# Kernel optimization log

Measured on AMD Instinct MI355X. Metric: run time of the kernel, lower is better.

The kernel has to match this reference:

```python
import jax, jax.numpy as jnp
import numpy as np
import math

B, C, N = 16, 512, 2048
MID = C // 2
EPS = 1e-5

def setup_inputs() -> dict:
    key = jax.random.key(0)
    ks = jax.random.split(key, 16)
    s = 0.02
    return {
        "x": jax.random.normal(ks[0], (B, C, N), jnp.float32),
        "wq": jax.random.normal(ks[1], (MID, C), jnp.float32) * s,
        "bq": jnp.zeros((MID,), jnp.float32),
        "gq": jnp.ones((MID,), jnp.float32),
        "betaq": jnp.zeros((MID,), jnp.float32),
        "wk": jax.random.normal(ks[2], (MID, C), jnp.float32) * s,
        "bk": jnp.zeros((MID,), jnp.float32),
        "gk": jnp.ones((MID,), jnp.float32),
        "betak": jnp.zeros((MID,), jnp.float32),
        "wv": jax.random.normal(ks[3], (MID, C), jnp.float32) * s,
        "bv": jnp.zeros((MID,), jnp.float32),
        "wo": jax.random.normal(ks[4], (C, MID), jnp.float32) * s,
        "bo": jnp.zeros((C,), jnp.float32),
        "mq": jnp.zeros((MID,), jnp.float32),
        "vq": jnp.ones((MID,), jnp.float32),
        "mk": jnp.zeros((MID,), jnp.float32),
        "vk": jnp.ones((MID,), jnp.float32),
    }

def _proj(x, w, b):
    # 1x1 Conv1d == per-position linear: [mid, C] x [B, C, N] -> [B, mid, N]
    return jnp.einsum('mc,bcn->bmn', w, x) + b[None, :, None]

def _bn_relu(z, gamma, beta, mean, var):
    # eval-mode BatchNorm1d over channel axis, then ReLU
    inv = gamma / jnp.sqrt(var + EPS)
    return jax.nn.relu(z * inv[None, :, None] + (beta - mean * inv)[None, :, None])

def reference(x, wq, bq, gq, betaq, wk, bk, gk, betak, wv, bv, wo, bo, mq, vq, mk, vk):
    q = _bn_relu(_proj(x, wq, bq), gq, betaq, mq, vq)   # [B, mid, N]
    k = _bn_relu(_proj(x, wk, bk), gk, betak, mk, vk)   # [B, mid, N]
    v = _proj(x, wv, bv)                                # [B, mid, N]
    scores = jnp.einsum('bmi,bmj->bij', q, k) / math.sqrt(MID)  # [B, Nq, Nk]
    attn = jax.nn.softmax(scores, axis=1)               # softmax over QUERY axis (dim=1)
    ctx = jnp.einsum('bci,bij->bcj', v, attn)           # [B, mid, N]
    out = jnp.einsum('cm,bmn->bcn', wo, ctx) + bo[None, :, None]
    return x + out
```

## Files before the change

### kernel.cpp

```cpp
#include <hip/hip_runtime.h>
#include <hip/hip_bf16.h>

#define B_ 16
#define C_ 512
#define N_ 2048
#define MID_ 256
#define EPS_ 1e-5f

typedef __attribute__((ext_vector_type(8))) short bf16x8;
typedef __attribute__((ext_vector_type(4))) float f32x4;
typedef __attribute__((ext_vector_type(8))) unsigned short us8;
typedef __attribute__((ext_vector_type(4))) unsigned short us4;

static __device__ __forceinline__ float bf2f(unsigned short u) {
    union { unsigned int i; float f; } c; c.i = ((unsigned int)u) << 16; return c.f;
}
static __device__ __forceinline__ unsigned short f2bf(float f) {
    __hip_bfloat16 h = __float2bfloat16(f);
    return *reinterpret_cast<unsigned short*>(&h);
}
static __device__ __forceinline__ us8 pack8(float4 a, float4 b) {
    us8 r;
    r[0] = f2bf(a.x); r[1] = f2bf(a.y); r[2] = f2bf(a.z); r[3] = f2bf(a.w);
    r[4] = f2bf(b.x); r[5] = f2bf(b.y); r[6] = f2bf(b.z); r[7] = f2bf(b.w);
    return r;
}

__global__ __launch_bounds__(256) void prep_x_kernel(
    const float* __restrict__ x, unsigned short* __restrict__ xt)
{
    const int b  = blockIdx.z;
    const int c0 = blockIdx.y * 64;
    const int n0 = blockIdx.x * 64;
    __shared__ unsigned short Ts[64][72];

    const int tid = threadIdx.x;
    const int cc  = tid >> 2;
    const int cq  = (tid & 3) * 4;

    #pragma unroll
    for (int i = 0; i < 4; i++) {
        float4 f = *(const float4*)&x[((size_t)b * C_ + c0 + cc) * N_ + n0 + cq + 16 * i];
        Ts[cq + 16 * i + 0][cc] = f2bf(f.x);
        Ts[cq + 16 * i + 1][cc] = f2bf(f.y);
        Ts[cq + 16 * i + 2][cc] = f2bf(f.z);
        Ts[cq + 16 * i + 3][cc] = f2bf(f.w);
    }
    __syncthreads();

    const int nn = tid >> 2;
    const int cg = (tid & 3) * 16;
    #pragma unroll
    for (int i = 0; i < 2; i++)
        *(us8*)&xt[((size_t)b * N_ + n0 + nn) * C_ + c0 + cg + 8 * i] =
            *(const us8*)&Ts[nn][cg + 8 * i];
}

__global__ __launch_bounds__(256) void prep_w_kernel(
    const float* __restrict__ wq, const float* __restrict__ wk,
    const float* __restrict__ wv, unsigned short* __restrict__ wb)
{
    const int nthr = gridDim.x * 256;
    for (int u = blockIdx.x * 256 + threadIdx.x; u < 98304; u += nthr) {
        int p = u >> 15;
        int o4 = u & 32767;
        const float* src = (p == 0) ? wq : (p == 1) ? wk : wv;
        float4 f = *(const float4*)&src[o4 * 4];
        us4 r;
        r[0] = f2bf(f.x); r[1] = f2bf(f.y); r[2] = f2bf(f.z); r[3] = f2bf(f.w);
        *(us4*)&wb[(size_t)p * 131072 + o4 * 4] = r;
    }
}

__global__ __launch_bounds__(256) void qkv_gemm_kernel(
    const unsigned short* __restrict__ xt, const unsigned short* __restrict__ wb,
    const float* __restrict__ bq, const float* __restrict__ gq,
    const float* __restrict__ betaq, const float* __restrict__ mq,
    const float* __restrict__ vq,
    const float* __restrict__ bk, const float* __restrict__ gk,
    const float* __restrict__ betak, const float* __restrict__ mk,
    const float* __restrict__ vk,
    const float* __restrict__ bv,
    unsigned short* __restrict__ qt, unsigned short* __restrict__ kt,
    unsigned short* __restrict__ v)
{
    const int p  = blockIdx.z % 3;
    const int b  = blockIdx.z / 3;
    const int n0 = blockIdx.x * 128;
    const int m0 = blockIdx.y * 128;

    __shared__ unsigned short Ws[128][72];
    __shared__ unsigned short Xs[128][72];
    __shared__ float sc_s[128], of_s[128];

    const int tid  = threadIdx.x;
    const int wave = tid >> 6;
    const int lane = tid & 63;
    const int quad = lane >> 4;
    const int l16  = lane & 15;
    const int wi   = wave >> 1;
    const int wj   = wave & 1;

    const unsigned short* wbp = wb + (size_t)p * 131072;
    const unsigned short* xtb = xt + (size_t)b * N_ * C_;

    if (tid < 128) {
        int m = m0 + tid;
        if (p == 0) {
            float inv = gq[m] * rsqrtf(vq[m] + EPS_);
            sc_s[tid] = inv * 0.0625f;
            of_s[tid] = ((bq[m] - mq[m]) * inv + betaq[m]) * 0.0625f;
        } else if (p == 1) {
            float inv = gk[m] * rsqrtf(vk[m] + EPS_);
            sc_s[tid] = inv; of_s[tid] = (bk[m] - mk[m]) * inv + betak[m];
        } else {
            sc_s[tid] = 1.0f; of_s[tid] = bv[m];
        }
    }

    unsigned short (*Asrc)[72] = (p == 2) ? Xs : Ws;
    unsigned short (*Bsrc)[72] = (p == 2) ? Ws : Xs;

    f32x4 acc[4][4];
    #pragma unroll
    for (int it = 0; it < 4; it++)
        #pragma unroll
        for (int jt = 0; jt < 4; jt++)
            #pragma unroll
            for (int r = 0; r < 4; r++) acc[it][jt][r] = 0.0f;

    const int srow  = tid >> 1;
    const int shalf = (tid & 1) * 32;

    for (int k0 = 0; k0 < C_; k0 += 64) {
        __syncthreads();
        #pragma unroll
        for (int i = 0; i < 4; i++) {
            *(us8*)&Ws[srow][shalf + 8 * i] =
                *(const us8*)&wbp[(size_t)(m0 + srow) * C_ + k0 + shalf + 8 * i];
            *(us8*)&Xs[srow][shalf + 8 * i] =
                *(const us8*)&xtb[(size_t)(n0 + srow) * C_ + k0 + shalf + 8 * i];
        }
        __syncthreads();
        #pragma unroll
        for (int cl = 0; cl < 64; cl += 32) {
            bf16x8 af[4], bfr[4];
            #pragma unroll
            for (int t = 0; t < 4; t++)
                af[t] = *(const bf16x8*)&Asrc[wi * 64 + t * 16 + l16][cl + quad * 8];
            #pragma unroll
            for (int t = 0; t < 4; t++)
                bfr[t] = *(const bf16x8*)&Bsrc[wj * 64 + t * 16 + l16][cl + quad * 8];
            #pragma unroll
            for (int it = 0; it < 4; it++)
                #pragma unroll
                for (int jt = 0; jt < 4; jt++)
                    acc[it][jt] = __builtin_amdgcn_mfma_f32_16x16x32_bf16(
                        af[it], bfr[jt], acc[it][jt], 0, 0, 0);
        }
    }
    __syncthreads();

    if (p < 2) {
        unsigned short* outT = (p == 0) ? qt : kt;
        #pragma unroll
        for (int it = 0; it < 4; it++) {
            int ml = wi * 64 + it * 16 + quad * 4;
            #pragma unroll
            for (int jt = 0; jt < 4; jt++) {
                int n = n0 + wj * 64 + jt * 16 + l16;
                us4 pk;
                #pragma unroll
                for (int r = 0; r < 4; r++) {
                    float val = acc[it][jt][r] * sc_s[ml + r] + of_s[ml + r];
                    pk[r] = f2bf(fmaxf(val, 0.0f));
                }
                *(us4*)&outT[((size_t)b * N_ + n) * MID_ + m0 + ml] = pk;
            }
        }
    } else {
        #pragma unroll
        for (int it = 0; it < 4; it++) {
            int nl = n0 + wi * 64 + it * 16 + quad * 4;
            #pragma unroll
            for (int jt = 0; jt < 4; jt++) {
                int mloc = wj * 64 + jt * 16 + l16;
                float off = of_s[mloc];
                us4 pk;
                #pragma unroll
                for (int r = 0; r < 4; r++)
                    pk[r] = f2bf(acc[it][jt][r] + off);
                *(us4*)&v[((size_t)b * MID_ + m0 + mloc) * N_ + nl] = pk;
            }
        }
    }
}

__global__ __launch_bounds__(256) void flash_kernel(
    const unsigned short* __restrict__ qt,
    const unsigned short* __restrict__ kt,
    const unsigned short* __restrict__ v,
    unsigned short* __restrict__ ctxT)
{
    const int b  = blockIdx.y;
    const int j0 = blockIdx.x * 64;

    __shared__ unsigned short Ks[64][264];
    __shared__ unsigned short Ps[64][72];
    __shared__ float red[4][64];

    const int tid  = threadIdx.x;
    const int wave = tid >> 6;
    const int lane = tid & 63;
    const int quad = lane >> 4;
    const int l16  = lane & 15;

    const unsigned short* qb = qt + (size_t)b * N_ * MID_;
    const unsigned short* kb = kt + (size_t)b * N_ * MID_;
    const unsigned short* vb = v  + (size_t)b * MID_ * N_;

    #pragma unroll
    for (int r = 0; r < 8; r++) {
        int ch = tid + r * 256;
        int j = ch >> 5, c8 = ch & 31;
        *(us8*)&Ks[j][c8 * 8] = *(const us8*)&kb[(size_t)(j0 + j) * MID_ + c8 * 8];
    }
    __syncthreads();

    f32x4 O[4][4];
    #pragma unroll
    for (int ct = 0; ct < 4; ct++)
        #pragma unroll
        for (int jt = 0; jt < 4; jt++)
            #pragma unroll
            for (int r = 0; r < 4; r++) O[ct][jt][r] = 0.0f;
    float psum[4] = {0.0f, 0.0f, 0.0f, 0.0f};

    const unsigned short* qbase = qb + (size_t)(wave * 16 + l16) * MID_ + quad * 8;
    const unsigned short* vbase = vb + (size_t)(wave * 64 + l16) * N_ + quad * 8;

    for (int i0 = 0; i0 < N_; i0 += 64) {
        f32x4 S[4];
        #pragma unroll
        for (int jt = 0; jt < 4; jt++)
            #pragma unroll
            for (int r = 0; r < 4; r++) S[jt][r] = 0.0f;

        const unsigned short* qp = qbase + (size_t)i0 * MID_;
        #pragma unroll
        for (int cc = 0; cc < MID_; cc += 32) {
            bf16x8 a = *(const bf16x8*)(qp + cc);
            #pragma unroll
            for (int jt = 0; jt < 4; jt++) {
                bf16x8 bf = *(const bf16x8*)&Ks[jt * 16 + l16][cc + quad * 8];
                S[jt] = __builtin_amdgcn_mfma_f32_16x16x32_bf16(a, bf, S[jt], 0, 0, 0);
            }
        }

        __syncthreads();
        #pragma unroll
        for (int jt = 0; jt < 4; jt++) {
            us4 pk;
            #pragma unroll
            for (int r = 0; r < 4; r++) {
                float e = __expf(S[jt][r]);
                psum[jt] += e;
                pk[r] = f2bf(e);
            }
            *(us4*)&Ps[jt * 16 + l16][wave * 16 + quad * 4] = pk;
        }
        __syncthreads();

        #pragma unroll
        for (int ic = 0; ic < 64; ic += 32) {
            bf16x8 pb[4];
            #pragma unroll
            for (int jt = 0; jt < 4; jt++)
                pb[jt] = *(const bf16x8*)&Ps[jt * 16 + l16][ic + quad * 8];
            #pragma unroll
            for (int ct = 0; ct < 4; ct++) {
                bf16x8 av = *(const bf16x8*)(vbase + (size_t)(ct * 16) * N_ + i0 + ic);
                #pragma unroll
                for (int jt = 0; jt < 4; jt++)
                    O[ct][jt] = __builtin_amdgcn_mfma_f32_16x16x32_bf16(
                        av, pb[jt], O[ct][jt], 0, 0, 0);
            }
        }
    }

    #pragma unroll
    for (int jt = 0; jt < 4; jt++) {
        psum[jt] += __shfl_xor(psum[jt], 16, 64);
        psum[jt] += __shfl_xor(psum[jt], 32, 64);
    }
    __syncthreads();
    if (quad == 0)
        #pragma unroll
        for (int jt = 0; jt < 4; jt++) red[wave][jt * 16 + l16] = psum[jt];
    __syncthreads();

    float rl[4];
    #pragma unroll
    for (int jt = 0; jt < 4; jt++)
        rl[jt] = 1.0f / (red[0][jt * 16 + l16] + red[1][jt * 16 + l16] +
                         red[2][jt * 16 + l16] + red[3][jt * 16 + l16]);

    #pragma unroll
    for (int ct = 0; ct < 4; ct++) {
        #pragma unroll
        for (int jt = 0; jt < 4; jt++) {
            us4 pk;
            #pragma unroll
            for (int r = 0; r < 4; r++)
                pk[r] = f2bf(O[ct][jt][r] * rl[jt]);
            int j = j0 + jt * 16 + l16;
            *(us4*)&ctxT[((size_t)b * N_ + j) * MID_ + wave * 64 + ct * 16 + quad * 4] = pk;
        }
    }
}

__global__ __launch_bounds__(256) void out_gemm_kernel(
    const float* __restrict__ wo, const float* __restrict__ bo,
    const unsigned short* __restrict__ ctxT, const float* __restrict__ x,
    float* __restrict__ out)
{
    const int b   = blockIdx.z;
    const int n0  = blockIdx.x * 128;
    const int co0 = blockIdx.y * 128;

    __shared__ unsigned short Wos[128][72];
    __shared__ unsigned short Cs[128][72];
    __shared__ float bo_s[128];

    const int tid  = threadIdx.x;
    const int wave = tid >> 6;
    const int lane = tid & 63;
    const int quad = lane >> 4;
    const int l16  = lane & 15;
    const int wi   = wave >> 1;
    const int wj   = wave & 1;

    if (tid < 128) bo_s[tid] = bo[co0 + tid];

    f32x4 acc[4][4];
    #pragma unroll
    for (int it = 0; it < 4; it++)
        #pragma unroll
        for (int jt = 0; jt < 4; jt++)
            #pragma unroll
            for (int r = 0; r < 4; r++) acc[it][jt][r] = 0.0f;

    const int srow  = tid >> 1;
    const int shalf = (tid & 1) * 32;

    for (int k0 = 0; k0 < MID_; k0 += 64) {
        __syncthreads();
        #pragma unroll
        for (int i = 0; i < 4; i++) {
            float4 f0 = *(const float4*)&wo[(size_t)(co0 + srow) * MID_ + k0 + shalf + 8 * i];
            float4 f1 = *(const float4*)&wo[(size_t)(co0 + srow) * MID_ + k0 + shalf + 8 * i + 4];
            *(us8*)&Wos[srow][shalf + 8 * i] = pack8(f0, f1);
            *(us8*)&Cs[srow][shalf + 8 * i] =
                *(const us8*)&ctxT[((size_t)b * N_ + n0 + srow) * MID_ + k0 + shalf + 8 * i];
        }
        __syncthreads();
        #pragma unroll
        for (int cl = 0; cl < 64; cl += 32) {
            bf16x8 af[4], bfr[4];
            #pragma unroll
            for (int t = 0; t < 4; t++)
                af[t] = *(const bf16x8*)&Wos[wi * 64 + t * 16 + l16][cl + quad * 8];
            #pragma unroll
            for (int t = 0; t < 4; t++)
                bfr[t] = *(const bf16x8*)&Cs[wj * 64 + t * 16 + l16][cl + quad * 8];
            #pragma unroll
            for (int it = 0; it < 4; it++)
                #pragma unroll
                for (int jt = 0; jt < 4; jt++)
                    acc[it][jt] = __builtin_amdgcn_mfma_f32_16x16x32_bf16(
                        af[it], bfr[jt], acc[it][jt], 0, 0, 0);
        }
    }
    __syncthreads();

    #pragma unroll
    for (int it = 0; it < 4; it++) {
        #pragma unroll
        for (int r = 0; r < 4; r++) {
            int col = wi * 64 + it * 16 + quad * 4 + r;
            int co = co0 + col;
            float bias = bo_s[col];
            #pragma unroll
            for (int jt = 0; jt < 4; jt++) {
                int n = n0 + wj * 64 + jt * 16 + l16;
                size_t a = ((size_t)b * C_ + co) * N_ + n;
                out[a] = acc[it][jt][r] + bias + x[a];
            }
        }
    }
}

extern "C" void kernel_launch(void* const* d_in, const int* in_sizes, int n_in,
                              void* d_out, int out_size, void* d_ws, size_t ws_size,
                              hipStream_t stream) {
    const float* x     = (const float*)d_in[0];
    const float* wq    = (const float*)d_in[1];
    const float* bq    = (const float*)d_in[2];
    const float* gq    = (const float*)d_in[3];
    const float* betaq = (const float*)d_in[4];
    const float* wk    = (const float*)d_in[5];
    const float* bk    = (const float*)d_in[6];
    const float* gk    = (const float*)d_in[7];
    const float* betak = (const float*)d_in[8];
    const float* wv    = (const float*)d_in[9];
    const float* bv    = (const float*)d_in[10];
    const float* wo    = (const float*)d_in[11];
    const float* bo    = (const float*)d_in[12];
    const float* mq    = (const float*)d_in[13];
    const float* vq    = (const float*)d_in[14];
    const float* mk    = (const float*)d_in[15];
    const float* vk    = (const float*)d_in[16];
    float* out = (float*)d_out;

    const size_t elems = (size_t)B_ * MID_ * N_;
    unsigned short* qt   = (unsigned short*)d_ws;
    unsigned short* kt   = qt + elems;
    unsigned short* v    = kt + elems;
    unsigned short* ctxT = v + elems;

    unsigned short* xt = (unsigned short*)d_out;
    unsigned short* wb = xt + (size_t)B_ * N_ * C_;

    prep_x_kernel<<<dim3(N_ / 64, C_ / 64, B_), 256, 0, stream>>>(x, xt);
    prep_w_kernel<<<dim3(96), 256, 0, stream>>>(wq, wk, wv, wb);

    qkv_gemm_kernel<<<dim3(N_ / 128, MID_ / 128, B_ * 3), 256, 0, stream>>>(
        xt, wb, bq, gq, betaq, mq, vq, bk, gk, betak, mk, vk, bv, qt, kt, v);

    flash_kernel<<<dim3(N_ / 64, B_), 256, 0, stream>>>(qt, kt, v, ctxT);

    out_gemm_kernel<<<dim3(N_ / 128, C_ / 128, B_), 256, 0, stream>>>(
        wo, bo, ctxT, x, out);
}
```

Before: 385.9 us.

## Double-buffer P tile and cache half of K fragments in registers in flash kernel

The flash attention loop is software-pipelined: the P tile in shared memory is double-buffered, so the PV MFMAs for tile t run before the QK and exp work for tile t+1, and only one barrier per iteration remains instead of two. Half of the K fragments are also held in registers for the whole kernel to cut LDS reads, and launch bounds request two blocks per CU. The extra 64 VGPRs for the cached K fragments, together with the occupancy hint, may force register spills or lower occupancy.

```diff
diff --git a/kernel.cpp b/kernel.cpp
--- a/kernel.cpp
+++ b/kernel.cpp
@@ -196,7 +196,7 @@
     }
 }
 
-__global__ __launch_bounds__(256) void flash_kernel(
+__global__ __launch_bounds__(256, 2) void flash_kernel(
     const unsigned short* __restrict__ qt,
     const unsigned short* __restrict__ kt,
     const unsigned short* __restrict__ v,
@@ -206,7 +206,7 @@
     const int j0 = blockIdx.x * 64;
 
     __shared__ unsigned short Ks[64][264];
-    __shared__ unsigned short Ps[64][72];
+    __shared__ unsigned short Ps[2][64][72];
     __shared__ float red[4][64];
 
     const int tid  = threadIdx.x;
@@ -227,6 +227,13 @@
     }
     __syncthreads();
 
+    bf16x8 kc[2][8];
+    #pragma unroll
+    for (int jt = 0; jt < 2; jt++)
+        #pragma unroll
+        for (int c = 0; c < 8; c++)
+            kc[jt][c] = *(const bf16x8*)&Ks[jt * 16 + l16][c * 32 + quad * 8];
+
     f32x4 O[4][4];
     #pragma unroll
     for (int ct = 0; ct < 4; ct++)
@@ -239,25 +246,23 @@
     const unsigned short* qbase = qb + (size_t)(wave * 16 + l16) * MID_ + quad * 8;
     const unsigned short* vbase = vb + (size_t)(wave * 64 + l16) * N_ + quad * 8;
 
-    for (int i0 = 0; i0 < N_; i0 += 64) {
+    {
         f32x4 S[4];
         #pragma unroll
         for (int jt = 0; jt < 4; jt++)
             #pragma unroll
             for (int r = 0; r < 4; r++) S[jt][r] = 0.0f;
 
-        const unsigned short* qp = qbase + (size_t)i0 * MID_;
-        #pragma unroll
-        for (int cc = 0; cc < MID_; cc += 32) {
-            bf16x8 a = *(const bf16x8*)(qp + cc);
-            #pragma unroll
-            for (int jt = 0; jt < 4; jt++) {
-                bf16x8 bf = *(const bf16x8*)&Ks[jt * 16 + l16][cc + quad * 8];
-                S[jt] = __builtin_amdgcn_mfma_f32_16x16x32_bf16(a, bf, S[jt], 0, 0, 0);
-            }
-        }
-
-        __syncthreads();
+        #pragma unroll
+        for (int c = 0; c < 8; c++) {
+            bf16x8 a = *(const bf16x8*)(qbase + c * 32);
+            S[0] = __builtin_amdgcn_mfma_f32_16x16x32_bf16(a, kc[0][c], S[0], 0, 0, 0);
+            S[1] = __builtin_amdgcn_mfma_f32_16x16x32_bf16(a, kc[1][c], S[1], 0, 0, 0);
+            bf16x8 b2 = *(const bf16x8*)&Ks[32 + l16][c * 32 + quad * 8];
+            S[2] = __builtin_amdgcn_mfma_f32_16x16x32_bf16(a, b2, S[2], 0, 0, 0);
+            bf16x8 b3 = *(const bf16x8*)&Ks[48 + l16][c * 32 + quad * 8];
+            S[3] = __builtin_amdgcn_mfma_f32_16x16x32_bf16(a, b3, S[3], 0, 0, 0);
+        }
         #pragma unroll
         for (int jt = 0; jt < 4; jt++) {
             us4 pk;
@@ -267,16 +272,71 @@
                 psum[jt] += e;
                 pk[r] = f2bf(e);
             }
-            *(us4*)&Ps[jt * 16 + l16][wave * 16 + quad * 4] = pk;
-        }
-        __syncthreads();
+            *(us4*)&Ps[0][jt * 16 + l16][wave * 16 + quad * 4] = pk;
+        }
+    }
+    __syncthreads();
+
+    for (int t = 0; t < 31; t++) {
+        const int i0  = t * 64;
+        const int buf = t & 1;
 
         #pragma unroll
         for (int ic = 0; ic < 64; ic += 32) {
             bf16x8 pb[4];
             #pragma unroll
             for (int jt = 0; jt < 4; jt++)
-                pb[jt] = *(const bf16x8*)&Ps[jt * 16 + l16][ic + quad * 8];
+                pb[jt] = *(const bf16x8*)&Ps[buf][jt * 16 + l16][ic + quad * 8];
+            #pragma unroll
+            for (int ct = 0; ct < 4; ct++) {
+                bf16x8 av = *(const bf16x8*)(vbase + (size_t)(ct * 16) * N_ + i0 + ic);
+                #pragma unroll
+                for (int jt = 0; jt < 4; jt++)
+                    O[ct][jt] = __builtin_amdgcn_mfma_f32_16x16x32_bf16(
+                        av, pb[jt], O[ct][jt], 0, 0, 0);
+            }
+        }
+
+        f32x4 S[4];
+        #pragma unroll
+        for (int jt = 0; jt < 4; jt++)
+            #pragma unroll
+            for (int r = 0; r < 4; r++) S[jt][r] = 0.0f;
+
+        const unsigned short* qp = qbase + (size_t)(i0 + 64) * MID_;
+        #pragma unroll
+        for (int c = 0; c < 8; c++) {
+            bf16x8 a = *(const bf16x8*)(qp + c * 32);
+            S[0] = __builtin_amdgcn_mfma_f32_16x16x32_bf16(a, kc[0][c], S[0], 0, 0, 0);
+            S[1] = __builtin_amdgcn_mfma_f32_16x16x32_bf16(a, kc[1][c], S[1], 0, 0, 0);
+            bf16x8 b2 = *(const bf16x8*)&Ks[32 + l16][c * 32 + quad * 8];
+            S[2] = __builtin_amdgcn_mfma_f32_16x16x32_bf16(a, b2, S[2], 0, 0, 0);
+            bf16x8 b3 = *(const bf16x8*)&Ks[48 + l16][c * 32 + quad * 8];
+            S[3] = __builtin_amdgcn_mfma_f32_16x16x32_bf16(a, b3, S[3], 0, 0, 0);
+        }
+
+        #pragma unroll
+        for (int jt = 0; jt < 4; jt++) {
+            us4 pk;
+            #pragma unroll
+            for (int r = 0; r < 4; r++) {
+                float e = __expf(S[jt][r]);
+                psum[jt] += e;
+                pk[r] = f2bf(e);
+            }
+            *(us4*)&Ps[buf ^ 1][jt * 16 + l16][wave * 16 + quad * 4] = pk;
+        }
+        __syncthreads();
+    }
+
+    {
+        const int i0 = 31 * 64;
+        #pragma unroll
+        for (int ic = 0; ic < 64; ic += 32) {
+            bf16x8 pb[4];
+            #pragma unroll
+            for (int jt = 0; jt < 4; jt++)
+                pb[jt] = *(const bf16x8*)&Ps[31 & 1][jt * 16 + l16][ic + quad * 8];
             #pragma unroll
             for (int ct = 0; ct < 4; ct++) {
                 bf16x8 av = *(const bf16x8*)(vbase + (size_t)(ct * 16) * N_ + i0 + ic);
```

Measured after the change: 381.3 us. No clear change (-1.2%).

## Software-pipeline flash kernel with double-buffered P tile and register prefetch

Applied to the files above, without the earlier changes.

Restructures the attention loop so the P·V accumulation for the current 64-row tile is interleaved with the QK^T score computation for the next tile. The P tile in shared memory is double-buffered, and V and Q fragments for the next tile are prefetched into registers. Two syncthreads per iteration become one lgkmcnt wait plus barrier. This is meant to hide global load latency and barrier stalls. In exchange it raises register pressure (launch_bounds 256,2) and risks spills.

```diff
diff --git a/kernel.cpp b/kernel.cpp
--- a/kernel.cpp
+++ b/kernel.cpp
@@ -196,7 +196,69 @@
     }
 }
 
-__global__ __launch_bounds__(256) void flash_kernel(
+#define LGKM_BARRIER() do { \
+    asm volatile("s_waitcnt lgkmcnt(0)" ::: "memory"); \
+    __builtin_amdgcn_s_barrier(); \
+} while (0)
+
+#define REGION(R, VC, VN) do { \
+    const int i0_ = (R) * 64; \
+     \
+    _Pragma("unroll") \
+    for (int u_ = 0; u_ < 8; u_++) \
+        VN[u_] = *(const bf16x8*)(vbase + (size_t)((u_ >> 1) * 16) * N_ + \
+                                  i0_ + 64 + (u_ & 1) * 32); \
+     \
+    _Pragma("unroll") \
+    for (int c_ = 0; c_ < 8; c_++) \
+        qf[c_] = *(const bf16x8*)(qbase + (size_t)(i0_ + 64) * MID_ + c_ * 32); \
+    __builtin_amdgcn_sched_barrier(0); \
+     \
+    _Pragma("unroll") \
+    for (int ic_ = 0; ic_ < 64; ic_ += 32) { \
+        bf16x8 pb[4]; \
+        _Pragma("unroll") \
+        for (int jt_ = 0; jt_ < 4; jt_++) \
+            pb[jt_] = *(const bf16x8*)&Ps[(R) & 1][jt_ * 16 + l16][ic_ + quad * 8]; \
+        _Pragma("unroll") \
+        for (int ct_ = 0; ct_ < 4; ct_++) { \
+            _Pragma("unroll") \
+            for (int jt_ = 0; jt_ < 4; jt_++) \
+                O[ct_][jt_] = __builtin_amdgcn_mfma_f32_16x16x32_bf16( \
+                    VC[ct_ * 2 + (ic_ >> 5)], pb[jt_], O[ct_][jt_], 0, 0, 0); \
+        } \
+    } \
+     \
+    f32x4 S[4]; \
+    _Pragma("unroll") \
+    for (int jt_ = 0; jt_ < 4; jt_++) \
+        _Pragma("unroll") \
+        for (int r_ = 0; r_ < 4; r_++) S[jt_][r_] = 0.0f; \
+    _Pragma("unroll") \
+    for (int c_ = 0; c_ < 8; c_++) { \
+        bf16x8 a_ = qf[c_]; \
+        _Pragma("unroll") \
+        for (int jt_ = 0; jt_ < 4; jt_++) { \
+            bf16x8 b_ = *(const bf16x8*)&Ks[jt_ * 16 + l16][c_ * 32 + quad * 8]; \
+            S[jt_] = __builtin_amdgcn_mfma_f32_16x16x32_bf16(a_, b_, S[jt_], 0, 0, 0); \
+        } \
+    } \
+     \
+    _Pragma("unroll") \
+    for (int jt_ = 0; jt_ < 4; jt_++) { \
+        us4 pk; \
+        _Pragma("unroll") \
+        for (int r_ = 0; r_ < 4; r_++) { \
+            float e_ = __expf(S[jt_][r_]); \
+            psum[jt_] += e_; \
+            pk[r_] = f2bf(e_); \
+        } \
+        *(us4*)&Ps[((R) & 1) ^ 1][jt_ * 16 + l16][wave * 16 + quad * 4] = pk; \
+    } \
+    LGKM_BARRIER(); \
+} while (0)
+
+__global__ __launch_bounds__(256, 2) void flash_kernel(
     const unsigned short* __restrict__ qt,
     const unsigned short* __restrict__ kt,
     const unsigned short* __restrict__ v,
@@ -206,7 +268,7 @@
     const int j0 = blockIdx.x * 64;
 
     __shared__ unsigned short Ks[64][264];
-    __shared__ unsigned short Ps[64][72];
+    __shared__ unsigned short Ps[2][64][72];
     __shared__ float red[4][64];
 
     const int tid  = threadIdx.x;
@@ -225,7 +287,6 @@
         int j = ch >> 5, c8 = ch & 31;
         *(us8*)&Ks[j][c8 * 8] = *(const us8*)&kb[(size_t)(j0 + j) * MID_ + c8 * 8];
     }
-    __syncthreads();
 
     f32x4 O[4][4];
     #pragma unroll
@@ -239,25 +300,34 @@
     const unsigned short* qbase = qb + (size_t)(wave * 16 + l16) * MID_ + quad * 8;
     const unsigned short* vbase = vb + (size_t)(wave * 64 + l16) * N_ + quad * 8;
 
-    for (int i0 = 0; i0 < N_; i0 += 64) {
+    bf16x8 vA[8], vB[8], qf[8];
+
+    bf16x8 q0[8];
+    #pragma unroll
+    for (int c = 0; c < 8; c++)
+        q0[c] = *(const bf16x8*)(qbase + c * 32);
+    #pragma unroll
+    for (int u = 0; u < 8; u++)
+        vA[u] = *(const bf16x8*)(vbase + (size_t)((u >> 1) * 16) * N_ + (u & 1) * 32);
+
+    LGKM_BARRIER();
+
+    {
         f32x4 S[4];
         #pragma unroll
         for (int jt = 0; jt < 4; jt++)
             #pragma unroll
             for (int r = 0; r < 4; r++) S[jt][r] = 0.0f;
 
-        const unsigned short* qp = qbase + (size_t)i0 * MID_;
-        #pragma unroll
-        for (int cc = 0; cc < MID_; cc += 32) {
-            bf16x8 a = *(const bf16x8*)(qp + cc);
+        #pragma unroll
+        for (int c = 0; c < 8; c++) {
+            bf16x8 a = q0[c];
             #pragma unroll
             for (int jt = 0; jt < 4; jt++) {
-                bf16x8 bf = *(const bf16x8*)&Ks[jt * 16 + l16][cc + quad * 8];
-                S[jt] = __builtin_amdgcn_mfma_f32_16x16x32_bf16(a, bf, S[jt], 0, 0, 0);
+                bf16x8 bfr = *(const bf16x8*)&Ks[jt * 16 + l16][c * 32 + quad * 8];
+                S[jt] = __builtin_amdgcn_mfma_f32_16x16x32_bf16(a, bfr, S[jt], 0, 0, 0);
             }
         }
-
-        __syncthreads();
         #pragma unroll
         for (int jt = 0; jt < 4; jt++) {
             us4 pk;
@@ -267,23 +337,30 @@
                 psum[jt] += e;
                 pk[r] = f2bf(e);
             }
-            *(us4*)&Ps[jt * 16 + l16][wave * 16 + quad * 4] = pk;
-        }
-        __syncthreads();
-
+            *(us4*)&Ps[0][jt * 16 + l16][wave * 16 + quad * 4] = pk;
+        }
+    }
+    LGKM_BARRIER();
+
+    for (int r = 0; r < 30; r += 2) {
+        REGION(r,     vA, vB);
+        REGION(r + 1, vB, vA);
+    }
+    REGION(30, vA, vB);
+
+    {
         #pragma unroll
         for (int ic = 0; ic < 64; ic += 32) {
             bf16x8 pb[4];
             #pragma unroll
             for (int jt = 0; jt < 4; jt++)
-                pb[jt] = *(const bf16x8*)&Ps[jt * 16 + l16][ic + quad * 8];
+                pb[jt] = *(const bf16x8*)&Ps[1][jt * 16 + l16][ic + quad * 8];
             #pragma unroll
             for (int ct = 0; ct < 4; ct++) {
-                bf16x8 av = *(const bf16x8*)(vbase + (size_t)(ct * 16) * N_ + i0 + ic);
                 #pragma unroll
                 for (int jt = 0; jt < 4; jt++)
                     O[ct][jt] = __builtin_amdgcn_mfma_f32_16x16x32_bf16(
-                        av, pb[jt], O[ct][jt], 0, 0, 0);
+                        vB[ct * 2 + (ic >> 5)], pb[jt], O[ct][jt], 0, 0, 0);
             }
         }
     }
```

After: 397.5 us. +3.0%, slower.

## Restructure flash kernel into 16-wave blocks with double-buffered P and 32x32 MFMA

Applied to the files above, without the earlier changes.

Rewrites the attention kernel to use 1024-thread blocks of 16 waves. Each block processes a 256-row query tile per step using 32x32x16 bf16 MFMAs. The P tile is double-buffered in shared memory so the score/exp of the next tile overlaps the PV accumulation of the current one, leaving one barrier per step instead of two. It also swizzles block IDs so blocks sharing a batch are spread across XCDs. The trade-off is much larger LDS use per block and higher register pressure under the launch bounds, which may limit occupancy.

```diff
diff --git a/kernel.cpp b/kernel.cpp
--- a/kernel.cpp
+++ b/kernel.cpp
@@ -9,6 +9,7 @@
 
 typedef __attribute__((ext_vector_type(8))) short bf16x8;
 typedef __attribute__((ext_vector_type(4))) float f32x4;
+typedef __attribute__((ext_vector_type(16))) float f32x16;
 typedef __attribute__((ext_vector_type(8))) unsigned short us8;
 typedef __attribute__((ext_vector_type(4))) unsigned short us4;
 
@@ -196,126 +197,143 @@
     }
 }
 
-__global__ __launch_bounds__(256) void flash_kernel(
+__global__ __launch_bounds__(1024, 4) void flash_kernel(
     const unsigned short* __restrict__ qt,
     const unsigned short* __restrict__ kt,
     const unsigned short* __restrict__ v,
     unsigned short* __restrict__ ctxT)
 {
-    const int b  = blockIdx.y;
-    const int j0 = blockIdx.x * 64;
-
-    __shared__ unsigned short Ks[64][264];
-    __shared__ unsigned short Ps[64][72];
-    __shared__ float red[4][64];
+    const int bid = blockIdx.x;
+    const int swz = (bid & 7) * 64 + (bid >> 3);
+    const int b   = swz >> 5;
+    const int j0  = (swz & 31) * 64;
+
+    __shared__ unsigned short Ks[64][272];
+    __shared__ unsigned short Ps[2][64][272];
+    __shared__ float red[8][64];
 
     const int tid  = threadIdx.x;
     const int wave = tid >> 6;
     const int lane = tid & 63;
-    const int quad = lane >> 4;
-    const int l16  = lane & 15;
+    const int l31  = lane & 31;
+    const int q5   = lane >> 5;
+    const int iw   = wave >> 1;
+    const int jt   = wave & 1;
 
     const unsigned short* qb = qt + (size_t)b * N_ * MID_;
     const unsigned short* kb = kt + (size_t)b * N_ * MID_;
     const unsigned short* vb = v  + (size_t)b * MID_ * N_;
 
     #pragma unroll
-    for (int r = 0; r < 8; r++) {
-        int ch = tid + r * 256;
+    for (int r = 0; r < 2; r++) {
+        int ch = tid + r * 1024;
         int j = ch >> 5, c8 = ch & 31;
         *(us8*)&Ks[j][c8 * 8] = *(const us8*)&kb[(size_t)(j0 + j) * MID_ + c8 * 8];
     }
     __syncthreads();
 
-    f32x4 O[4][4];
-    #pragma unroll
-    for (int ct = 0; ct < 4; ct++)
-        #pragma unroll
-        for (int jt = 0; jt < 4; jt++)
-            #pragma unroll
-            for (int r = 0; r < 4; r++) O[ct][jt][r] = 0.0f;
-    float psum[4] = {0.0f, 0.0f, 0.0f, 0.0f};
-
-    const unsigned short* qbase = qb + (size_t)(wave * 16 + l16) * MID_ + quad * 8;
-    const unsigned short* vbase = vb + (size_t)(wave * 64 + l16) * N_ + quad * 8;
-
-    for (int i0 = 0; i0 < N_; i0 += 64) {
-        f32x4 S[4];
-        #pragma unroll
-        for (int jt = 0; jt < 4; jt++)
-            #pragma unroll
-            for (int r = 0; r < 4; r++) S[jt][r] = 0.0f;
-
-        const unsigned short* qp = qbase + (size_t)i0 * MID_;
-        #pragma unroll
-        for (int cc = 0; cc < MID_; cc += 32) {
-            bf16x8 a = *(const bf16x8*)(qp + cc);
-            #pragma unroll
-            for (int jt = 0; jt < 4; jt++) {
-                bf16x8 bf = *(const bf16x8*)&Ks[jt * 16 + l16][cc + quad * 8];
-                S[jt] = __builtin_amdgcn_mfma_f32_16x16x32_bf16(a, bf, S[jt], 0, 0, 0);
-            }
-        }
-
+    f32x16 O;
+    #pragma unroll
+    for (int r = 0; r < 16; r++) O[r] = 0.0f;
+    float psum = 0.0f;
+
+    const unsigned short* qrow0 = qb + (size_t)(iw * 32 + l31) * MID_ + q5 * 8;
+    const unsigned short* vrow  = vb + (size_t)(iw * 32 + l31) * N_  + q5 * 8;
+    const unsigned short* kp    = &Ks[jt * 32 + l31][q5 * 8];
+    unsigned short* pw          = &Ps[0][jt * 32 + l31][iw * 32 + q5 * 4];
+    const unsigned short* pr    = &Ps[0][jt * 32 + l31][q5 * 8];
+    const size_t psz = (size_t)64 * 272;
+
+    {
+        f32x16 S1;
+        #pragma unroll
+        for (int r = 0; r < 16; r++) S1[r] = 0.0f;
+        #pragma unroll
+        for (int ks = 0; ks < 16; ks++) {
+            bf16x8 aq = *(const bf16x8*)(qrow0 + ks * 16);
+            bf16x8 bk = *(const bf16x8*)(kp + ks * 16);
+            S1 = __builtin_amdgcn_mfma_f32_32x32x16_bf16(aq, bk, S1, 0, 0, 0);
+        }
+        #pragma unroll
+        for (int g = 0; g < 4; g++) {
+            us4 pk;
+            #pragma unroll
+            for (int r = 0; r < 4; r++) {
+                float e = __expf(S1[g * 4 + r]);
+                psum += e;
+                pk[r] = f2bf(e);
+            }
+            *(us4*)(pw + g * 8) = pk;
+        }
+    }
+    __syncthreads();
+
+    for (int t = 0; t < 7; t++) {
+        const int i0   = t * 256;
+        const int buf  = t & 1;
+        const int nbuf = buf ^ 1;
+
+        {
+            f32x16 S1;
+            #pragma unroll
+            for (int r = 0; r < 16; r++) S1[r] = 0.0f;
+            const unsigned short* qrow = qrow0 + (size_t)(i0 + 256) * MID_;
+            #pragma unroll
+            for (int ks = 0; ks < 16; ks++) {
+                bf16x8 aq = *(const bf16x8*)(qrow + ks * 16);
+                bf16x8 bk = *(const bf16x8*)(kp + ks * 16);
+                S1 = __builtin_amdgcn_mfma_f32_32x32x16_bf16(aq, bk, S1, 0, 0, 0);
+            }
+            #pragma unroll
+            for (int g = 0; g < 4; g++) {
+                us4 pk;
+                #pragma unroll
+                for (int r = 0; r < 4; r++) {
+                    float e = __expf(S1[g * 4 + r]);
+                    psum += e;
+                    pk[r] = f2bf(e);
+                }
+                *(us4*)(pw + (size_t)nbuf * psz + g * 8) = pk;
+            }
+        }
+
+        #pragma unroll
+        for (int ks = 0; ks < 16; ks++) {
+            bf16x8 av = *(const bf16x8*)(vrow + i0 + ks * 16);
+            bf16x8 pb = *(const bf16x8*)(pr + (size_t)buf * psz + ks * 16);
+            O = __builtin_amdgcn_mfma_f32_32x32x16_bf16(av, pb, O, 0, 0, 0);
+        }
         __syncthreads();
-        #pragma unroll
-        for (int jt = 0; jt < 4; jt++) {
-            us4 pk;
-            #pragma unroll
-            for (int r = 0; r < 4; r++) {
-                float e = __expf(S[jt][r]);
-                psum[jt] += e;
-                pk[r] = f2bf(e);
-            }
-            *(us4*)&Ps[jt * 16 + l16][wave * 16 + quad * 4] = pk;
-        }
-        __syncthreads();
-
-        #pragma unroll
-        for (int ic = 0; ic < 64; ic += 32) {
-            bf16x8 pb[4];
-            #pragma unroll
-            for (int jt = 0; jt < 4; jt++)
-                pb[jt] = *(const bf16x8*)&Ps[jt * 16 + l16][ic + quad * 8];
-            #pragma unroll
-            for (int ct = 0; ct < 4; ct++) {
-                bf16x8 av = *(const bf16x8*)(vbase + (size_t)(ct * 16) * N_ + i0 + ic);
-                #pragma unroll
-                for (int jt = 0; jt < 4; jt++)
-                    O[ct][jt] = __builtin_amdgcn_mfma_f32_16x16x32_bf16(
-                        av, pb[jt], O[ct][jt], 0, 0, 0);
-            }
-        }
-    }
-
-    #pragma unroll
-    for (int jt = 0; jt < 4; jt++) {
-        psum[jt] += __shfl_xor(psum[jt], 16, 64);
-        psum[jt] += __shfl_xor(psum[jt], 32, 64);
-    }
-    __syncthreads();
-    if (quad == 0)
-        #pragma unroll
-        for (int jt = 0; jt < 4; jt++) red[wave][jt * 16 + l16] = psum[jt];
-    __syncthreads();
-
-    float rl[4];
-    #pragma unroll
-    for (int jt = 0; jt < 4; jt++)
-        rl[jt] = 1.0f / (red[0][jt * 16 + l16] + red[1][jt * 16 + l16] +
-                         red[2][jt * 16 + l16] + red[3][jt * 16 + l16]);
-
-    #pragma unroll
-    for (int ct = 0; ct < 4; ct++) {
-        #pragma unroll
-        for (int jt = 0; jt < 4; jt++) {
-            us4 pk;
-            #pragma unroll
-            for (int r = 0; r < 4; r++)
-                pk[r] = f2bf(O[ct][jt][r] * rl[jt]);
-            int j = j0 + jt * 16 + l16;
-            *(us4*)&ctxT[((size_t)b * N_ + j) * MID_ + wave * 64 + ct * 16 + quad * 4] = pk;
-        }
+    }
+
+    {
+        const int i0 = 7 * 256;
+        #pragma unroll
+        for (int ks = 0; ks < 16; ks++) {
+            bf16x8 av = *(const bf16x8*)(vrow + i0 + ks * 16);
+            bf16x8 pb = *(const bf16x8*)(pr + psz + ks * 16);
+            O = __builtin_amdgcn_mfma_f32_32x32x16_bf16(av, pb, O, 0, 0, 0);
+        }
+    }
+
+    psum += __shfl_xor(psum, 32, 64);
+    if (lane < 32) red[wave >> 1][jt * 32 + lane] = psum;
+    __syncthreads();
+
+    float dsum = 0.0f;
+    #pragma unroll
+    for (int rr = 0; rr < 8; rr++) dsum += red[rr][jt * 32 + l31];
+    const float rl = 1.0f / dsum;
+
+    unsigned short* orow = ctxT + ((size_t)b * N_ + j0 + jt * 32 + l31) * MID_ +
+                           iw * 32 + q5 * 4;
+    #pragma unroll
+    for (int g = 0; g < 4; g++) {
+        us4 pk;
+        #pragma unroll
+        for (int r = 0; r < 4; r++)
+            pk[r] = f2bf(O[g * 4 + r] * rl);
+        *(us4*)(orow + g * 8) = pk;
     }
 }
 
@@ -437,7 +455,7 @@
     qkv_gemm_kernel<<<dim3(N_ / 128, MID_ / 128, B_ * 3), 256, 0, stream>>>(
         xt, wb, bq, gq, betaq, mq, vq, bk, gk, betak, mk, vk, bv, qt, kt, v);
 
-    flash_kernel<<<dim3(N_ / 64, B_), 256, 0, stream>>>(qt, kt, v, ctxT);
+    flash_kernel<<<dim3(512), 1024, 0, stream>>>(qt, kt, v, ctxT);
 
     out_gemm_kernel<<<dim3(N_ / 128, C_ / 128, B_), 256, 0, stream>>>(
         wo, bo, ctxT, x, out);
```

Measured after the change: 485.4 us. +25.8%, slower.
